# Optimization experiments

Hardware: AMD Instinct MI355X
Metric: run time of the kernel (lower is better)

Reference implementation:

```python
import jax, jax.numpy as jnp
import numpy as np

B, K, S, H, V, T = 32, 5, 64, 768, 30522, 40
SEP = 102


def setup_inputs() -> dict:
    key = jax.random.key(0)
    ks = jax.random.split(key, 8)
    s = 0.02
    return {
        "src": jax.random.normal(ks[0], (B, S, H), jnp.float32),
        "E": jax.random.normal(ks[1], (V, H), jnp.float32) * s,
        "Wa": jax.random.normal(ks[2], (H, H), jnp.float32) * s,
        "Ua": jax.random.normal(ks[3], (H, H), jnp.float32) * s,
        "va": jax.random.normal(ks[4], (H,), jnp.float32) * s,
        "W_ih": jax.random.normal(ks[5], (3 * H, 2 * H), jnp.float32) * s,
        "W_hh": jax.random.normal(ks[6], (3 * H, H), jnp.float32) * s,
        "b_ih": jnp.zeros((3 * H,), jnp.float32),
        "b_hh": jnp.zeros((3 * H,), jnp.float32),
        "Wo": jax.random.normal(ks[7], (V, H), jnp.float32) * s,
        "bo": jnp.zeros((V,), jnp.float32),
    }


def _decoder(tok, src, h, E, Wa, Ua, va, W_ih, W_hh, b_ih, b_hh, Wo, bo):
    # tok [N] int, src [N,S,H], h [N,H] -> (logits [N,V], h_new [N,H])
    emb = E[tok]                                              # [N,H]
    e = jnp.tanh(src @ Wa + (h @ Ua)[:, None, :]) @ va        # [N,S]
    a = jax.nn.softmax(e, axis=-1)
    ctx = jnp.einsum('ns,nsd->nd', a, src)                    # [N,H]
    x = jnp.concatenate([emb, ctx], axis=-1)                  # [N,2H]
    gx = x @ W_ih.T + b_ih
    gh = h @ W_hh.T + b_hh
    xr, xz, xn = jnp.split(gx, 3, axis=-1)
    hr, hz, hn = jnp.split(gh, 3, axis=-1)
    r = jax.nn.sigmoid(xr + hr)
    z = jax.nn.sigmoid(xz + hz)
    n = jnp.tanh(xn + r * hn)
    h2 = (1.0 - z) * n + z * h
    return h2 @ Wo.T + bo, h2


def _search(src, E, Wa, Ua, va, W_ih, W_hh, b_ih, b_hh, Wo, bo):
    P = (E, Wa, Ua, va, W_ih, W_hh, b_ih, b_hh, Wo, bo)
    # step 0: start token 102, zero hidden
    tok0 = jnp.full((B,), SEP, jnp.int32)
    logits, h = _decoder(tok0, src, jnp.zeros((B, H), src.dtype), *P)
    logp = jax.nn.log_softmax(logits, axis=-1)
    scores, toks = jax.lax.top_k(logp, K)                     # [B,K]
    hiddens = jnp.broadcast_to(h[:, None, :], (B, K, H))
    src_k = jnp.broadcast_to(src[:, None], (B, K, S, H)).reshape(B * K, S, H)
    no_prob = jnp.full((V,), -1e9, src.dtype).at[SEP].set(0.0)
    beam_mask = jnp.arange(K) < K - 1  # original normalizes only first k-1 segments

    def body(carry, _):
        toks, maps, hiddens, scores, ended, lengths = carry
        # parent hidden per beam (gather by backpointer), decode all beams at once
        h_in = jnp.take_along_axis(hiddens, maps[:, :, None], axis=1)  # [B,K,H]
        logits, h_new = _decoder(toks.reshape(-1), src_k, h_in.reshape(B * K, H), *P)
        logp = jax.nn.log_softmax(logits, axis=-1).reshape(B, K, V)
        logp = jnp.where(ended[:, :, None] == 0, logp, no_prob)
        lengths = lengths + (ended == 0).astype(lengths.dtype)
        cand = logp + scores[:, :, None]                      # [B,K,V]
        denom = jnp.where(beam_mask, lengths ** 0.7, 1.0)     # [B,K]
        norm = (cand / denom[:, :, None]).reshape(B, K * V)
        _, idx = jax.lax.top_k(norm, K)                       # [B,K]
        new_scores = jnp.take_along_axis(cand.reshape(B, K * V), idx, axis=1)
        new_toks = (idx % V).astype(jnp.int32)
        new_maps = (idx // V).astype(jnp.int32)
        ended = jnp.where(new_toks == SEP, 1.0, ended)
        new_carry = (new_toks, new_maps, h_new.reshape(B, K, H), new_scores, ended, lengths)
        return new_carry, (new_toks, new_maps)

    carry0 = (toks.astype(jnp.int32), jnp.zeros((B, K), jnp.int32), hiddens,
              scores, jnp.zeros((B, K), src.dtype), jnp.zeros((B, K), src.dtype))
    carryF, (toks_seq, maps_seq) = jax.lax.scan(body, carry0, None, length=T - 1)
    toks_all = jnp.concatenate([toks[None].astype(jnp.int32), toks_seq], axis=0)   # [T,B,K]
    maps_all = jnp.concatenate([jnp.zeros((1, B, K), jnp.int32), maps_seq], axis=0)
    final_scores = carryF[3]
    best = jnp.argmax(final_scores, axis=1).astype(jnp.int32)  # [B]

    def back(idx, tm):
        tk, mp = tm
        out = jnp.take_along_axis(tk, idx[:, None], axis=1)[:, 0]
        nxt = jnp.take_along_axis(mp, idx[:, None], axis=1)[:, 0]
        return nxt, out

    _, outs = jax.lax.scan(back, best, (toks_all, maps_all), reverse=True)
    return outs.T, final_scores  # tokens [B,T], scores [B,K]


def reference(src, E, Wa, Ua, va, W_ih, W_hh, b_ih, b_hh, Wo, bo):
    tokens, _ = _search(src, E, Wa, Ua, va, W_ih, W_hh, b_ih, b_hh, Wo, bo)
    return tokens
```

## Files before the change

kernel.cpp:

```cpp
#include <hip/hip_runtime.h>
#include <cmath>
#include <cfloat>

#define Hdim 768
#define Bb 32
#define Kb 5
#define Ss 64
#define Vv 30522
#define Tt 40
#define SEPTOK 102

template<int NT>
__global__ __launch_bounds__(256) void gemmT_k(int N, int P, int I, int xrs,
    long long sWp, long long sWi,
    const float* __restrict__ Xf, const float* __restrict__ W,
    const float* __restrict__ bias, float* __restrict__ out)
{
    __shared__ double xs[NT][256];
    int tid = threadIdx.x;
    int i0 = blockIdx.x * 512 + tid;
    int i1 = i0 + 256;
    int n0 = blockIdx.y * NT;
    long long i0c = (i0 < I) ? i0 : (I - 1);
    long long i1c = (i1 < I) ? i1 : (I - 1);
    double acc0[NT], acc1[NT];
#pragma unroll
    for (int r = 0; r < NT; r++) { acc0[r] = 0.0; acc1[r] = 0.0; }
    int nch = P >> 8;
    for (int c = 0; c < nch; c++) {
        __syncthreads();
        for (int idx = tid; idx < NT * 256; idx += 256) {
            int r = idx >> 8, p = idx & 255;
            xs[r][p] = (double)Xf[(size_t)(n0 + r) * xrs + c * 256 + p];
        }
        __syncthreads();
        const float* wrow = W + (size_t)c * 256 * sWp;
#pragma unroll 2
        for (int p = 0; p < 256; p++) {
            double w0 = (double)wrow[(size_t)p * sWp + i0c * sWi];
            double w1 = (double)wrow[(size_t)p * sWp + i1c * sWi];
#pragma unroll
            for (int r = 0; r < NT; r++) {
                double x = xs[r][p];
                acc0[r] = ::fma(x, w0, acc0[r]);
                acc1[r] = ::fma(x, w1, acc1[r]);
            }
        }
    }
    if (i0 < I) {
#pragma unroll
        for (int r = 0; r < NT; r++) {
            float s = (float)acc0[r];
            if (bias) s = __fadd_rn(s, bias[i0]);
            out[(size_t)(n0 + r) * I + i0] = s;
        }
    }
    if (i1 < I) {
#pragma unroll
        for (int r = 0; r < NT; r++) {
            float s = (float)acc1[r];
            if (bias) s = __fadd_rn(s, bias[i1]);
            out[(size_t)(n0 + r) * I + i1] = s;
        }
    }
}

__global__ __launch_bounds__(256) void transpose_tiled_k(
    const float* __restrict__ in, float* __restrict__ out, int R, int C)
{
    __shared__ float tile[32][33];
    int c0 = blockIdx.x * 32, r0 = blockIdx.y * 32;
    int tx = threadIdx.x & 31, ty = threadIdx.x >> 5;
    for (int dy = 0; dy < 32; dy += 8) {
        int r = r0 + ty + dy, c = c0 + tx;
        if (r < R && c < C) tile[ty + dy][tx] = in[(size_t)r * C + c];
    }
    __syncthreads();
    for (int dy = 0; dy < 32; dy += 8) {
        int r = r0 + tx, c = c0 + ty + dy;
        if (r < R && c < C) out[(size_t)c * R + r] = tile[tx][ty + dy];
    }
}

__global__ __launch_bounds__(256) void gather_k(int N, int Kcur,
    const int* __restrict__ maps, const int* __restrict__ toks,
    const float* __restrict__ h_beam, const float* __restrict__ E,
    float* __restrict__ h_g, float* __restrict__ xbuf)
{
    int n = blockIdx.x;
    if (n >= N) return;
    int b = n / Kcur;
    int tok = toks ? toks[n] : SEPTOK;
    const float* er = E + (size_t)tok * Hdim;
    if (maps) {
        const float* hs = h_beam + (size_t)(b * Kb + maps[n]) * Hdim;
        for (int j = threadIdx.x; j < Hdim; j += 256) {
            h_g[(size_t)n * Hdim + j]  = hs[j];
            xbuf[(size_t)n * 1536 + j] = er[j];
        }
    } else {
        for (int j = threadIdx.x; j < Hdim; j += 256) {
            h_g[(size_t)n * Hdim + j]  = 0.f;
            xbuf[(size_t)n * 1536 + j] = er[j];
        }
    }
}

__global__ __launch_bounds__(256) void bcast_k(const float* __restrict__ h_tmp,
                                               float* __restrict__ h_beam)
{
    int b = blockIdx.x;
    for (int j = threadIdx.x; j < Hdim; j += 256) {
        float v = h_tmp[(size_t)b * Hdim + j];
        for (int k = 0; k < Kb; k++)
            h_beam[(size_t)(b * Kb + k) * Hdim + j] = v;
    }
}

__global__ __launch_bounds__(256) void attn2_k(int N, int Kcur,
    const float* __restrict__ hUa, const float* __restrict__ srcWa,
    const float* __restrict__ src, const float* __restrict__ va,
    float* __restrict__ xbuf)
{
    __shared__ float hu[Hdim];
    __shared__ float va_s[Hdim];
    __shared__ float e_s[Ss];
    __shared__ float a_s[Ss];
    int n = blockIdx.x, tid = threadIdx.x;
    if (n >= N) return;
    int b = n / Kcur;
    for (int j = tid; j < Hdim; j += 256) {
        hu[j]   = hUa[(size_t)n * Hdim + j];
        va_s[j] = va[j];
    }
    __syncthreads();
    int wv = tid >> 6, ln = tid & 63;
    for (int s = wv * 16; s < wv * 16 + 16; s++) {
        const float* sw = srcWa + (size_t)(b * Ss + s) * Hdim;
        double p = 0.0;
        for (int j = ln; j < Hdim; j += 64) {
            float tv = (float)tanh((double)__fadd_rn(sw[j], hu[j]));
            p = ::fma((double)tv, (double)va_s[j], p);
        }
        for (int off = 32; off; off >>= 1) p += __shfl_down(p, off, 64);
        if (ln == 0) e_s[s] = (float)p;
    }
    __syncthreads();
    if (tid < 64) {
        float v = e_s[tid], m = v;
        for (int off = 32; off; off >>= 1) m = fmaxf(m, __shfl_xor(m, off, 64));
        float p = (float)exp((double)__fsub_rn(v, m));
        double sum = (double)p;
        for (int off = 32; off; off >>= 1) sum += __shfl_xor(sum, off, 64);
        a_s[tid] = __fdiv_rn(p, (float)sum);
    }
    __syncthreads();
    for (int j = tid; j < Hdim; j += 256) {
        double acc = 0.0;
        for (int s = 0; s < Ss; s++)
            acc = ::fma((double)a_s[s], (double)src[(size_t)(b * Ss + s) * Hdim + j], acc);
        xbuf[(size_t)n * 1536 + 768 + j] = (float)acc;
    }
}

__global__ __launch_bounds__(256) void gate_k(int N,
    const float* __restrict__ gx, const float* __restrict__ gh,
    const float* __restrict__ h_g, float* __restrict__ h_out)
{
    int idx = blockIdx.x * 256 + threadIdx.x;
    if (idx >= N * Hdim) return;
    int n = idx / Hdim, i = idx - n * Hdim;
    const float* gxr = gx + (size_t)n * 2304;
    const float* ghr = gh + (size_t)n * 2304;
    float xr = gxr[i], xz = gxr[768 + i], xn = gxr[1536 + i];
    float hr = ghr[i], hz = ghr[768 + i], hn = ghr[1536 + i];
    float r  = (float)(1.0 / (1.0 + exp(-(double)__fadd_rn(xr, hr))));
    float z  = (float)(1.0 / (1.0 + exp(-(double)__fadd_rn(xz, hz))));
    float nn = (float)tanh((double)__fadd_rn(xn, __fmul_rn(r, hn)));
    float hv = h_g[(size_t)n * Hdim + i];
    float h2 = __fadd_rn(__fmul_rn(__fsub_rn(1.f, z), nn), __fmul_rn(z, hv));
    h_out[(size_t)n * Hdim + i] = h2;
}

__global__ __launch_bounds__(256) void lse_k(int N,
    const float* __restrict__ logits, float* __restrict__ mx, float* __restrict__ lgs)
{
    __shared__ float  redf[256];
    __shared__ double redd[256];
    int n = blockIdx.x, tid = threadIdx.x;
    const float* lg = logits + (size_t)n * Vv;
    float m = -INFINITY;
    for (int v = tid; v < Vv; v += 256) m = fmaxf(m, lg[v]);
    redf[tid] = m; __syncthreads();
    for (int off = 128; off; off >>= 1) {
        if (tid < off) redf[tid] = fmaxf(redf[tid], redf[tid + off]);
        __syncthreads();
    }
    m = redf[0];
    double s = 0.0;
    for (int v = tid; v < Vv; v += 256) {
        float ex = (float)exp((double)__fsub_rn(lg[v], m));
        s += (double)ex;
    }
    redd[tid] = s; __syncthreads();
    for (int off = 128; off; off >>= 1) {
        if (tid < off) redd[tid] += redd[tid + off];
        __syncthreads();
    }
    if (tid == 0) {
        mx[n] = m;
        float sf = (float)redd[0];
        lgs[n] = (float)log((double)sf);
    }
}

__device__ __forceinline__ bool betterf(float va, int ja, float vb, int jb) {
    return (va > vb) || (va == vb && ja < jb);
}
__device__ __forceinline__ void ins5(float* tv, int* tj, float v, int j) {
    if (!betterf(v, j, tv[4], tj[4])) return;
    tv[4] = v; tj[4] = j;
#pragma unroll
    for (int q = 4; q > 0; q--) {
        if (betterf(tv[q], tj[q], tv[q - 1], tj[q - 1])) {
            float t = tv[q]; tv[q] = tv[q - 1]; tv[q - 1] = t;
            int  ti = tj[q]; tj[q] = tj[q - 1]; tj[q - 1] = ti;
        }
    }
}

__global__ __launch_bounds__(256) void topk5_k(int t,
    const float* __restrict__ logits, const float* __restrict__ mx, const float* __restrict__ lgs,
    float* scores, float* ended, float* lengths,
    int* toks_cur, int* maps_cur, int* toks_all, int* maps_all)
{
    __shared__ float sc_s[Kb], den_s[Kb], end_s[Kb], len_s[Kb], mx_s[Kb], lg_s[Kb];
    __shared__ float mv[256 * 5];
    __shared__ int   mj[256 * 5];
    __shared__ float rv[256];
    __shared__ int   rj[256];
    __shared__ int   selj[Kb];
    int b = blockIdx.x, tid = threadIdx.x;
    int Kcur = (t == 0) ? 1 : Kb;
    if (tid < Kb) {
        if (t == 0) {
            sc_s[tid] = 0.f; end_s[tid] = 0.f; len_s[tid] = 0.f; den_s[tid] = 1.f;
            mx_s[tid] = mx[b]; lg_s[tid] = lgs[b];
        } else {
            float e0 = ended[b * Kb + tid];
            float ln = __fadd_rn(lengths[b * Kb + tid], (e0 == 0.f) ? 1.f : 0.f);
            sc_s[tid]  = scores[b * Kb + tid];
            end_s[tid] = e0;
            len_s[tid] = ln;
            den_s[tid] = (tid < Kb - 1) ? (float)pow((double)ln, (double)0.7f) : 1.f;
            mx_s[tid]  = mx[b * Kb + tid];
            lg_s[tid]  = lgs[b * Kb + tid];
        }
    }
    __syncthreads();
    const float* lbase = logits + (size_t)b * Kcur * Vv;
    float tv[5]; int tj[5];
#pragma unroll
    for (int q = 0; q < 5; q++) { tv[q] = -INFINITY; tj[q] = 0x7fffffff; }
    for (int k = 0; k < Kcur; k++) {
        if (end_s[k] == 0.f) {
            float m = mx_s[k], l = lg_s[k], sck = sc_s[k], den = den_s[k];
            const float* lg = lbase + (size_t)k * Vv;
            for (int v = tid; v < Vv; v += 256) {
                float lp  = __fsub_rn(__fsub_rn(lg[v], m), l);
                float val = __fdiv_rn(__fadd_rn(lp, sck), den);
                ins5(tv, tj, val, k * Vv + v);
            }
        } else if (tid == 0) {
            float val = __fdiv_rn(sc_s[k], den_s[k]);
            ins5(tv, tj, val, k * Vv + SEPTOK);
        }
    }
#pragma unroll
    for (int q = 0; q < 5; q++) { mv[tid * 5 + q] = tv[q]; mj[tid * 5 + q] = tj[q]; }
    __syncthreads();
    for (int pass = 0; pass < Kb; pass++) {
        float bv = -INFINITY; int bj = 0x7fffffff;
#pragma unroll
        for (int q = 0; q < 5; q++) {
            float v = mv[tid * 5 + q]; int j = mj[tid * 5 + q];
            if (betterf(v, j, bv, bj)) { bv = v; bj = j; }
        }
        rv[tid] = bv; rj[tid] = bj;
        __syncthreads();
        for (int off = 128; off; off >>= 1) {
            if (tid < off) {
                float ov = rv[tid + off]; int oj = rj[tid + off];
                if (betterf(ov, oj, rv[tid], rj[tid])) { rv[tid] = ov; rj[tid] = oj; }
            }
            __syncthreads();
        }
        if (tid == 0) selj[pass] = rj[0];
        __syncthreads();
#pragma unroll
        for (int q = 0; q < 5; q++)
            if (mj[tid * 5 + q] == selj[pass]) { mv[tid * 5 + q] = -INFINITY; mj[tid * 5 + q] = 0x7fffffff; }
        __syncthreads();
    }
    if (tid == 0) {
        for (int q = 0; q < Kb; q++) {
            int jj = selj[q];
            int pk = jj / Vv, vv = jj - pk * Vv;
            float lp;
            if (end_s[pk] == 0.f)
                lp = __fsub_rn(__fsub_rn(lbase[(size_t)pk * Vv + vv], mx_s[pk]), lg_s[pk]);
            else
                lp = (vv == SEPTOK) ? 0.f : -1e9f;
            float cand = __fadd_rn(lp, sc_s[pk]);
            scores[b * Kb + q]   = cand;
            toks_cur[b * Kb + q] = vv;
            maps_cur[b * Kb + q] = (t == 0) ? 0 : pk;
            if (t == 0) {
                ended[b * Kb + q]   = 0.f;
                lengths[b * Kb + q] = 0.f;
            } else {
                ended[b * Kb + q]   = (vv == SEPTOK) ? 1.f : end_s[q];
                lengths[b * Kb + q] = len_s[q];
            }
            toks_all[(size_t)t * Bb * Kb + b * Kb + q] = vv;
            maps_all[(size_t)t * Bb * Kb + b * Kb + q] = (t == 0) ? 0 : pk;
        }
    }
}

__global__ void back_k(const float* __restrict__ scores,
                       const int* __restrict__ toks_all, const int* __restrict__ maps_all,
                       int* __restrict__ out)
{
    int b = threadIdx.x;
    if (b >= Bb) return;
    int best = 0; float bvv = scores[b * Kb];
    for (int k = 1; k < Kb; k++) {
        float v = scores[b * Kb + k];
        if (v > bvv) { bvv = v; best = k; }
    }
    int cur = best;
    for (int t = Tt - 1; t >= 0; t--) {
        out[b * Tt + t] = toks_all[t * Bb * Kb + b * Kb + cur];
        cur = maps_all[t * Bb * Kb + b * Kb + cur];
    }
}

extern "C" void kernel_launch(void* const* d_in, const int* in_sizes, int n_in,
                              void* d_out, int out_size, void* d_ws, size_t ws_size,
                              hipStream_t stream)
{
    const float* src  = (const float*)d_in[0];
    const float* E    = (const float*)d_in[1];
    const float* Wa   = (const float*)d_in[2];
    const float* Ua   = (const float*)d_in[3];
    const float* va   = (const float*)d_in[4];
    const float* W_ih = (const float*)d_in[5];
    const float* W_hh = (const float*)d_in[6];
    const float* b_ih = (const float*)d_in[7];
    const float* b_hh = (const float*)d_in[8];
    const float* Wo   = (const float*)d_in[9];
    const float* bo   = (const float*)d_in[10];
    int* out = (int*)d_out;

    char* w = (char*)d_ws;
    size_t used = 0;
    auto alloc = [&](size_t bytes) -> char* {
        char* p = w + used;
        used += (bytes + 255) & ~(size_t)255;
        return p;
    };
    float*  srcWa   = (float*) alloc((size_t)Bb * Ss * Hdim * 4);
    float*  h_beam  = (float*) alloc((size_t)Bb * Kb * Hdim * 4);
    float*  h_tmp   = (float*) alloc((size_t)Bb * Hdim * 4);
    float*  h_g     = (float*) alloc((size_t)Bb * Kb * Hdim * 4);
    float*  hUa     = (float*) alloc((size_t)Bb * Kb * Hdim * 4);
    float*  xbuf    = (float*) alloc((size_t)Bb * Kb * 1536 * 4);
    float*  gx      = (float*) alloc((size_t)Bb * Kb * 2304 * 4);
    float*  gh      = (float*) alloc((size_t)Bb * Kb * 2304 * 4);
    float*  logits  = (float*) alloc((size_t)Bb * Kb * Vv * 4);
    float*  mx      = (float*) alloc(Bb * Kb * 4);
    float*  lgs     = (float*) alloc(Bb * Kb * 4);
    float*  scores  = (float*) alloc(Bb * Kb * 4);
    float*  ended   = (float*) alloc(Bb * Kb * 4);
    float*  lengths = (float*) alloc(Bb * Kb * 4);
    int* toks_cur = (int*)alloc(Bb * Kb * 4);
    int* maps_cur = (int*)alloc(Bb * Kb * 4);
    int* toks_all = (int*)alloc((size_t)Tt * Bb * Kb * 4);
    int* maps_all = (int*)alloc((size_t)Tt * Bb * Kb * 4);

    size_t sz_ihT = (size_t)2304 * 1536 * 4;
    size_t sz_hhT = (size_t)2304 * Hdim * 4;
    size_t sz_woT = (size_t)Vv * Hdim * 4;
    float* wihT = nullptr; float* whhT = nullptr; float* woT = nullptr;
    if (ws_size >= used + sz_ihT + sz_hhT + 512) {
        wihT = (float*)alloc(sz_ihT);
        whhT = (float*)alloc(sz_hhT);
    }
    if (ws_size >= used + sz_woT + 512) {
        woT = (float*)alloc(sz_woT);
    }

    if (wihT) {
        transpose_tiled_k<<<dim3((1536 + 31) / 32, (2304 + 31) / 32), 256, 0, stream>>>(W_ih, wihT, 2304, 1536);
        transpose_tiled_k<<<dim3((Hdim + 31) / 32, (2304 + 31) / 32), 256, 0, stream>>>(W_hh, whhT, 2304, Hdim);
    }
    if (woT)
        transpose_tiled_k<<<dim3((Hdim + 31) / 32, (Vv + 31) / 32), 256, 0, stream>>>(Wo, woT, Vv, Hdim);

    gemmT_k<16><<<dim3(2, (Bb * Ss) / 16), 256, 0, stream>>>(
        Bb * Ss, Hdim, Hdim, Hdim, (long long)Hdim, 1LL, src, Wa, nullptr, srcWa);

    const float* Wih_p = wihT ? wihT : W_ih;
    long long    Wih_sp = wihT ? 2304LL : 1LL, Wih_si = wihT ? 1LL : 1536LL;
    const float* Whh_p = whhT ? whhT : W_hh;
    long long    Whh_sp = whhT ? 2304LL : 1LL, Whh_si = whhT ? 1LL : (long long)Hdim;
    const float* Wo_p  = woT ? woT : Wo;
    long long    Wo_sp = woT ? (long long)Vv : 1LL, Wo_si = woT ? 1LL : (long long)Hdim;

    for (int t = 0; t < Tt; t++) {
        int N  = (t == 0) ? Bb : Bb * Kb;
        int Kc = (t == 0) ? 1 : Kb;
        const int* mp = (t == 0) ? nullptr : maps_cur;
        const int* tk = (t == 0) ? nullptr : toks_cur;
        float* h_cur = (t == 0) ? h_tmp : h_beam;

        gather_k<<<N, 256, 0, stream>>>(N, Kc, mp, tk, h_beam, E, h_g, xbuf);
        gemmT_k<4><<<dim3(2, N / 4), 256, 0, stream>>>(
            N, Hdim, Hdim, Hdim, (long long)Hdim, 1LL, h_g, Ua, nullptr, hUa);
        attn2_k<<<N, 256, 0, stream>>>(N, Kc, hUa, srcWa, src, va, xbuf);
        gemmT_k<4><<<dim3(5, N / 4), 256, 0, stream>>>(
            N, 1536, 2304, 1536, Wih_sp, Wih_si, xbuf, Wih_p, b_ih, gx);
        gemmT_k<4><<<dim3(5, N / 4), 256, 0, stream>>>(
            N, Hdim, 2304, Hdim, Whh_sp, Whh_si, h_g, Whh_p, b_hh, gh);
        gate_k<<<(N * Hdim + 255) / 256, 256, 0, stream>>>(N, gx, gh, h_g, h_cur);
        if (t == 0)
            bcast_k<<<Bb, 256, 0, stream>>>(h_tmp, h_beam);
        gemmT_k<16><<<dim3(60, N / 16), 256, 0, stream>>>(
            N, Hdim, Vv, Hdim, Wo_sp, Wo_si, h_cur, Wo_p, bo, logits);
        lse_k<<<N, 256, 0, stream>>>(N, logits, mx, lgs);
        topk5_k<<<Bb, 256, 0, stream>>>(t, logits, mx, lgs, scores, ended, lengths,
                                        toks_cur, maps_cur, toks_all, maps_all);
    }
    back_k<<<1, 64, 0, stream>>>(scores, toks_all, maps_all, out);
}
```

Before: 53.28 ms.

## Replace GEMM kernel with LDS-tiled weight staging and drop weight transposes

Swaps the GEMM kernel, which read weights straight from global memory, for one that stages 16-wide K chunks of both activations and weights in shared memory. Each thread now accumulates 16 rows by 2 or 4 column groups in double precision. Weights are read in their native layout using vectorized loads, once per 16-row block, so the separate transpose kernels and their workspace are removed. The cost is a much larger per-thread accumulator array (up to 64 doubles), which raises register pressure and may lower occupancy. It also adds more syncs per K step.

```diff
diff --git a/kernel.cpp b/kernel.cpp
--- a/kernel.cpp
+++ b/kernel.cpp
@@ -9,76 +9,99 @@
 #define Vv 30522
 #define Tt 40
 #define SEPTOK 102
-
-template<int NT>
-__global__ __launch_bounds__(256) void gemmT_k(int N, int P, int I, int xrs,
-    long long sWp, long long sWi,
+#define PC 16
+
+typedef __attribute__((ext_vector_type(2))) double f64x2;
+typedef __attribute__((ext_vector_type(2))) float  f32x2;
+typedef __attribute__((ext_vector_type(4))) float  f32x4;
+
+template<int CPT, bool PMAJOR>
+__global__ __launch_bounds__(256) void gemmL_k(int P, int I, int xrs, int ld,
     const float* __restrict__ Xf, const float* __restrict__ W,
     const float* __restrict__ bias, float* __restrict__ out)
 {
-    __shared__ double xs[NT][256];
+    __shared__ double xs[16][18];
+    __shared__ float  wt[CPT * 256][18];
     int tid = threadIdx.x;
-    int i0 = blockIdx.x * 512 + tid;
-    int i1 = i0 + 256;
-    int n0 = blockIdx.y * NT;
-    long long i0c = (i0 < I) ? i0 : (I - 1);
-    long long i1c = (i1 < I) ? i1 : (I - 1);
-    double acc0[NT], acc1[NT];
-#pragma unroll
-    for (int r = 0; r < NT; r++) { acc0[r] = 0.0; acc1[r] = 0.0; }
-    int nch = P >> 8;
+    int n0 = blockIdx.y * 16;
+    int i0 = blockIdx.x * (CPT * 256);
+    double acc[CPT][16];
+#pragma unroll
+    for (int s = 0; s < CPT; s++)
+#pragma unroll
+        for (int r = 0; r < 16; r++) acc[s][r] = 0.0;
+
+    int nch = P / PC;
     for (int c = 0; c < nch; c++) {
-        __syncthreads();
-        for (int idx = tid; idx < NT * 256; idx += 256) {
-            int r = idx >> 8, p = idx & 255;
-            xs[r][p] = (double)Xf[(size_t)(n0 + r) * xrs + c * 256 + p];
-        }
-        __syncthreads();
-        const float* wrow = W + (size_t)c * 256 * sWp;
-#pragma unroll 2
-        for (int p = 0; p < 256; p++) {
-            double w0 = (double)wrow[(size_t)p * sWp + i0c * sWi];
-            double w1 = (double)wrow[(size_t)p * sWp + i1c * sWi];
-#pragma unroll
-            for (int r = 0; r < NT; r++) {
-                double x = xs[r][p];
-                acc0[r] = ::fma(x, w0, acc0[r]);
-                acc1[r] = ::fma(x, w1, acc1[r]);
-            }
-        }
-    }
-    if (i0 < I) {
-#pragma unroll
-        for (int r = 0; r < NT; r++) {
-            float s = (float)acc0[r];
-            if (bias) s = __fadd_rn(s, bias[i0]);
-            out[(size_t)(n0 + r) * I + i0] = s;
-        }
-    }
-    if (i1 < I) {
-#pragma unroll
-        for (int r = 0; r < NT; r++) {
-            float s = (float)acc1[r];
-            if (bias) s = __fadd_rn(s, bias[i1]);
-            out[(size_t)(n0 + r) * I + i1] = s;
-        }
-    }
-}
-
-__global__ __launch_bounds__(256) void transpose_tiled_k(
-    const float* __restrict__ in, float* __restrict__ out, int R, int C)
-{
-    __shared__ float tile[32][33];
-    int c0 = blockIdx.x * 32, r0 = blockIdx.y * 32;
-    int tx = threadIdx.x & 31, ty = threadIdx.x >> 5;
-    for (int dy = 0; dy < 32; dy += 8) {
-        int r = r0 + ty + dy, c = c0 + tx;
-        if (r < R && c < C) tile[ty + dy][tx] = in[(size_t)r * C + c];
-    }
-    __syncthreads();
-    for (int dy = 0; dy < 32; dy += 8) {
-        int r = r0 + tx, c = c0 + ty + dy;
-        if (r < R && c < C) out[(size_t)c * R + r] = tile[tx][ty + dy];
+        int p0 = c * PC;
+        __syncthreads();
+        {
+            int r = tid >> 4, p = tid & 15;
+            xs[r][p] = (double)Xf[(size_t)(n0 + r) * xrs + p0 + p];
+        }
+        if (PMAJOR) {
+            const int LPR = CPT * 64;
+            const int RPI = 256 / LPR;
+            int i4 = (tid % LPR) * 4;
+            int pl = tid / LPR;
+#pragma unroll
+            for (int it = 0; it < PC / RPI; ++it) {
+                int p = pl + it * RPI;
+                int gi = i0 + i4;
+                f32x4 v = {0.f, 0.f, 0.f, 0.f};
+                if (gi + 3 < I) {
+                    v = *(const f32x4*)&W[(size_t)(p0 + p) * ld + gi];
+                } else {
+#pragma unroll
+                    for (int q = 0; q < 4; q++)
+                        if (gi + q < I) v[q] = W[(size_t)(p0 + p) * ld + gi + q];
+                }
+                wt[i4 + 0][p] = v[0]; wt[i4 + 1][p] = v[1];
+                wt[i4 + 2][p] = v[2]; wt[i4 + 3][p] = v[3];
+            }
+        } else {
+            int p4 = (tid & 3) * 4;
+            int il = tid >> 2;
+#pragma unroll
+            for (int it = 0; it < CPT * 4; ++it) {
+                int i_loc = il + it * 64;
+                long long gi = i0 + i_loc;
+                if (gi >= I) gi = I - 1;
+                f32x4 v = *(const f32x4*)&W[(size_t)gi * ld + p0 + p4];
+                wt[i_loc][p4 + 0] = v[0]; wt[i_loc][p4 + 1] = v[1];
+                wt[i_loc][p4 + 2] = v[2]; wt[i_loc][p4 + 3] = v[3];
+            }
+        }
+        __syncthreads();
+#pragma unroll
+        for (int p2 = 0; p2 < PC; p2 += 2) {
+            f32x2 wv[CPT];
+#pragma unroll
+            for (int s = 0; s < CPT; s++)
+                wv[s] = *(const f32x2*)&wt[s * 256 + tid][p2];
+#pragma unroll
+            for (int r = 0; r < 16; r++) {
+                f64x2 xv = *(const f64x2*)&xs[r][p2];
+#pragma unroll
+                for (int s = 0; s < CPT; s++) {
+                    acc[s][r] = ::fma(xv.x, (double)wv[s].x, acc[s][r]);
+                    acc[s][r] = ::fma(xv.y, (double)wv[s].y, acc[s][r]);
+                }
+            }
+        }
+    }
+#pragma unroll
+    for (int s = 0; s < CPT; s++) {
+        int cs = i0 + s * 256 + tid;
+        if (cs < I) {
+            float bv = bias ? bias[cs] : 0.f;
+#pragma unroll
+            for (int r = 0; r < 16; r++) {
+                float v = (float)acc[s][r];
+                if (bias) v = __fadd_rn(v, bv);
+                out[(size_t)(n0 + r) * I + cs] = v;
+            }
+        }
     }
 }
 
@@ -389,34 +412,8 @@
     int* toks_all = (int*)alloc((size_t)Tt * Bb * Kb * 4);
     int* maps_all = (int*)alloc((size_t)Tt * Bb * Kb * 4);
 
-    size_t sz_ihT = (size_t)2304 * 1536 * 4;
-    size_t sz_hhT = (size_t)2304 * Hdim * 4;
-    size_t sz_woT = (size_t)Vv * Hdim * 4;
-    float* wihT = nullptr; float* whhT = nullptr; float* woT = nullptr;
-    if (ws_size >= used + sz_ihT + sz_hhT + 512) {
-        wihT = (float*)alloc(sz_ihT);
-        whhT = (float*)alloc(sz_hhT);
-    }
-    if (ws_size >= used + sz_woT + 512) {
-        woT = (float*)alloc(sz_woT);
-    }
-
-    if (wihT) {
-        transpose_tiled_k<<<dim3((1536 + 31) / 32, (2304 + 31) / 32), 256, 0, stream>>>(W_ih, wihT, 2304, 1536);
-        transpose_tiled_k<<<dim3((Hdim + 31) / 32, (2304 + 31) / 32), 256, 0, stream>>>(W_hh, whhT, 2304, Hdim);
-    }
-    if (woT)
-        transpose_tiled_k<<<dim3((Hdim + 31) / 32, (Vv + 31) / 32), 256, 0, stream>>>(Wo, woT, Vv, Hdim);
-
-    gemmT_k<16><<<dim3(2, (Bb * Ss) / 16), 256, 0, stream>>>(
-        Bb * Ss, Hdim, Hdim, Hdim, (long long)Hdim, 1LL, src, Wa, nullptr, srcWa);
-
-    const float* Wih_p = wihT ? wihT : W_ih;
-    long long    Wih_sp = wihT ? 2304LL : 1LL, Wih_si = wihT ? 1LL : 1536LL;
-    const float* Whh_p = whhT ? whhT : W_hh;
-    long long    Whh_sp = whhT ? 2304LL : 1LL, Whh_si = whhT ? 1LL : (long long)Hdim;
-    const float* Wo_p  = woT ? woT : Wo;
-    long long    Wo_sp = woT ? (long long)Vv : 1LL, Wo_si = woT ? 1LL : (long long)Hdim;
+    gemmL_k<2, true><<<dim3(2, (Bb * Ss) / 16), 256, 0, stream>>>(
+        Hdim, Hdim, Hdim, Hdim, src, Wa, nullptr, srcWa);
 
     for (int t = 0; t < Tt; t++) {
         int N  = (t == 0) ? Bb : Bb * Kb;
@@ -424,20 +421,21 @@
         const int* mp = (t == 0) ? nullptr : maps_cur;
         const int* tk = (t == 0) ? nullptr : toks_cur;
         float* h_cur = (t == 0) ? h_tmp : h_beam;
+        int nrt = N / 16;
 
         gather_k<<<N, 256, 0, stream>>>(N, Kc, mp, tk, h_beam, E, h_g, xbuf);
-        gemmT_k<4><<<dim3(2, N / 4), 256, 0, stream>>>(
-            N, Hdim, Hdim, Hdim, (long long)Hdim, 1LL, h_g, Ua, nullptr, hUa);
+        gemmL_k<2, true><<<dim3(2, nrt), 256, 0, stream>>>(
+            Hdim, Hdim, Hdim, Hdim, h_g, Ua, nullptr, hUa);
         attn2_k<<<N, 256, 0, stream>>>(N, Kc, hUa, srcWa, src, va, xbuf);
-        gemmT_k<4><<<dim3(5, N / 4), 256, 0, stream>>>(
-            N, 1536, 2304, 1536, Wih_sp, Wih_si, xbuf, Wih_p, b_ih, gx);
-        gemmT_k<4><<<dim3(5, N / 4), 256, 0, stream>>>(
-            N, Hdim, 2304, Hdim, Whh_sp, Whh_si, h_g, Whh_p, b_hh, gh);
+        gemmL_k<2, false><<<dim3(5, nrt), 256, 0, stream>>>(
+            1536, 2304, 1536, 1536, xbuf, W_ih, b_ih, gx);
+        gemmL_k<2, false><<<dim3(5, nrt), 256, 0, stream>>>(
+            Hdim, 2304, Hdim, Hdim, h_g, W_hh, b_hh, gh);
         gate_k<<<(N * Hdim + 255) / 256, 256, 0, stream>>>(N, gx, gh, h_g, h_cur);
         if (t == 0)
             bcast_k<<<Bb, 256, 0, stream>>>(h_tmp, h_beam);
-        gemmT_k<16><<<dim3(60, N / 16), 256, 0, stream>>>(
-            N, Hdim, Vv, Hdim, Wo_sp, Wo_si, h_cur, Wo_p, bo, logits);
+        gemmL_k<4, false><<<dim3(30, nrt), 256, 0, stream>>>(
+            Hdim, Vv, Hdim, Hdim, h_cur, Wo, bo, logits);
         lse_k<<<N, 256, 0, stream>>>(N, logits, mx, lgs);
         topk5_k<<<Bb, 256, 0, stream>>>(t, logits, mx, lgs, scores, ended, lengths,
                                         toks_cur, maps_cur, toks_all, maps_all);
```

New measurement: 107.7 ms. 102% more time.
